# Kernel tuning notes

Hardware: AMD Instinct MI355X
Metric: run time of the kernel (lower is better)

## Reference

```python
import jax, jax.numpy as jnp
import numpy as np

NUM_USER, NUM_ITEM, K, B = 8192, 16384, 2048, 2048
LAMD0, CC, P = 40000.0, 5000.0, 0.5


def setup_inputs() -> dict:
    key = jax.random.key(0)
    ks = jax.random.split(key, 11)
    UI = (jax.random.uniform(ks[0], (NUM_USER, NUM_ITEM)) < 0.02).astype(jnp.float32)
    u = jax.random.normal(ks[1], (NUM_ITEM, K), dtype=jnp.float32) * 0.02
    s = jax.random.uniform(ks[2], (K,), dtype=jnp.float32) * 100.0 + 1.0  # positive singular values
    vh = jax.random.normal(ks[3], (K, NUM_ITEM), dtype=jnp.float32) * 0.02
    lamd_w = jnp.zeros((K, 1), jnp.float32)
    D_w = jnp.zeros((NUM_ITEM, 1), jnp.float32)
    Db_w = jnp.zeros((1, NUM_ITEM), jnp.float32)
    # dropout mask with keep prob 1-P, scaled by 1/(1-P) (torch training-mode Dropout)
    drop_mask = (jax.random.uniform(ks[4], (B, NUM_ITEM)) > P).astype(jnp.float32) / (1.0 - P)
    user = jax.random.randint(ks[5], (B,), 0, NUM_USER)
    pos_item = jax.random.randint(ks[6], (B,), 0, NUM_ITEM)
    neg_item = jax.random.randint(ks[7], (B,), 0, NUM_ITEM)
    return {"UI": UI, "u": u, "s": s, "vh": vh, "lamd_w": lamd_w, "D_w": D_w,
            "Db_w": Db_w, "drop_mask": drop_mask, "user": user,
            "pos_item": pos_item, "neg_item": neg_item}


def _gather_W_cols(u, ss, vh, dg, dbg, items):
    # Columns of W = sigmoid(D) * (u @ diag(ss) @ vh) * sigmoid(Db), diag zeroed.
    # Equivalent to original getW() followed by W[:, items], without materializing W.
    cols = u @ (ss[:, None] * vh[:, items])          # [num_item, Bi]
    cols = dg[:, None] * cols * dbg[items][None, :]  # row gate * col gate
    cols = cols.at[items, jnp.arange(items.shape[0])].set(0.0)  # W[i,i] = 0
    return cols.T                                    # [Bi, num_item]


def reference(UI, u, s, vh, lamd_w, D_w, Db_w, drop_mask, user, pos_item, neg_item):
    ss = s / (s + LAMD0 + CC * jnp.tanh(lamd_w[:, 0]))  # [K]
    dg = jax.nn.sigmoid(D_w[:, 0])    # [num_item] row gate
    dbg = jax.nn.sigmoid(Db_w[0])     # [num_item] col gate
    posW = _gather_W_cols(u, ss, vh, dg, dbg, pos_item)  # [B, num_item]
    negW = _gather_W_cols(u, ss, vh, dg, dbg, neg_item)  # [B, num_item]
    A = UI[user]                                          # [B, num_item]
    A = A.at[jnp.arange(user.shape[0]), pos_item].set(0.0)
    A = A * drop_mask
    pos = (A * posW).sum(1)
    neg = (A * negW).sum(1)
    loss = -jax.nn.log_sigmoid(100.0 * (pos - neg)).mean()
    return loss
```

## Files before the change

### kernel.cpp

```cpp
#include <hip/hip_runtime.h>
#include <hip/hip_bf16.h>
#include <math.h>

#define NUSER 8192
#define NITEM 16384
#define KD 2048
#define BB 2048

typedef __bf16 bf16;
typedef __bf16 bf16x8 __attribute__((ext_vector_type(8)));
typedef float f32x4 __attribute__((ext_vector_type(4)));

__global__ __launch_bounds__(256) void gates_kernel(
    const float* __restrict__ s, const float* __restrict__ lamd_w,
    const float* __restrict__ D_w, const float* __restrict__ Db_w,
    float* __restrict__ ss, float* __restrict__ dg, float* __restrict__ dbg) {
  int i = blockIdx.x * 256 + threadIdx.x;
  if (i < NITEM) {
    dg[i] = 1.0f / (1.0f + expf(-D_w[i]));
    dbg[i] = 1.0f / (1.0f + expf(-Db_w[i]));
    if (i < KD) {
      float sv = s[i];
      ss[i] = sv / (sv + 40000.0f + 5000.0f * tanhf(lamd_w[i]));
    }
  }
}

__global__ __launch_bounds__(256) void prep_a_kernel(
    const float* __restrict__ UI, const float* __restrict__ drop,
    const float* __restrict__ dg, const int* __restrict__ user,
    const int* __restrict__ pos_item, bf16* __restrict__ Ag) {
  int j = blockIdx.x;
  int t = threadIdx.x;
  int uj = user[j];
  int pj = pos_item[j];
  const float* uirow = UI + (size_t)uj * NITEM;
  const float* drow = drop + (size_t)j * NITEM;
  bf16* arow = Ag + (size_t)j * NITEM;
#pragma unroll
  for (int it = 0; it < 8; ++it) {
    int i = it * 2048 + t * 8;
    float4 a0 = *(const float4*)&uirow[i];
    float4 a1 = *(const float4*)&uirow[i + 4];
    float4 d0 = *(const float4*)&drow[i];
    float4 d1 = *(const float4*)&drow[i + 4];
    float4 g0 = *(const float4*)&dg[i];
    float4 g1 = *(const float4*)&dg[i + 4];
    float v[8] = {a0.x * d0.x * g0.x, a0.y * d0.y * g0.y, a0.z * d0.z * g0.z,
                  a0.w * d0.w * g0.w, a1.x * d1.x * g1.x, a1.y * d1.y * g1.y,
                  a1.z * d1.z * g1.z, a1.w * d1.w * g1.w};
    bf16x8 o;
#pragma unroll
    for (int w = 0; w < 8; ++w) o[w] = (bf16)((i + w == pj) ? 0.0f : v[w]);
    *(bf16x8*)&arow[i] = o;
  }
}

__global__ __launch_bounds__(256) void transpose_u_kernel(
    const float* __restrict__ u, bf16* __restrict__ Bt) {
  __shared__ bf16 ldsT[64][72];
  int i0 = blockIdx.x * 64;
  int k0 = blockIdx.y * 64;
  int t = threadIdx.x;
  int r = t >> 2, q = t & 3;
#pragma unroll
  for (int cc = 0; cc < 4; ++cc) {
    int col = q * 16 + cc * 4;
    float4 v = *(const float4*)&u[(size_t)(i0 + r) * KD + k0 + col];
    ldsT[col + 0][r] = (bf16)v.x;
    ldsT[col + 1][r] = (bf16)v.y;
    ldsT[col + 2][r] = (bf16)v.z;
    ldsT[col + 3][r] = (bf16)v.w;
  }
  __syncthreads();
#pragma unroll
  for (int g = 0; g < 2; ++g) {
    int ii = q * 16 + g * 8;
    bf16x8 v = *(const bf16x8*)&ldsT[r][ii];
    *(bf16x8*)&Bt[(size_t)(k0 + r) * NITEM + i0 + ii] = v;
  }
}

#define BM 128
#define BN 128
#define BKK 64

__global__ __launch_bounds__(256) void gemm_kernel(
    const bf16* __restrict__ A, const bf16* __restrict__ Bt,
    float* __restrict__ Y) {
  __shared__ bf16 lA[BM][BKK + 8];
  __shared__ bf16 lB[BN][BKK + 8];
  int bm = blockIdx.x * BM;
  int bn = blockIdx.y * BN;
  int kz = blockIdx.z;
  int tid = threadIdx.x;
  int wid = tid >> 6, lane = tid & 63;
  int wr = (wid >> 1) * 64, wc = (wid & 1) * 64;
  int lrow = lane & 15;
  int lko = (lane >> 4) * 8;
  f32x4 acc[4][4] = {};
  int kbeg = kz * (NITEM / 4), kend = kbeg + NITEM / 4;
  for (int kt = kbeg; kt < kend; kt += BKK) {
#pragma unroll
    for (int it = 0; it < 4; ++it) {
      int idx = tid + it * 256;
      int rr = idx >> 3, c8 = (idx & 7) * 8;
      *(bf16x8*)&lA[rr][c8] = *(const bf16x8*)&A[(size_t)(bm + rr) * NITEM + kt + c8];
      *(bf16x8*)&lB[rr][c8] = *(const bf16x8*)&Bt[(size_t)(bn + rr) * NITEM + kt + c8];
    }
    __syncthreads();
#pragma unroll
    for (int kk = 0; kk < BKK; kk += 32) {
      bf16x8 af[4], bfv[4];
#pragma unroll
      for (int m = 0; m < 4; ++m) af[m] = *(const bf16x8*)&lA[wr + m * 16 + lrow][kk + lko];
#pragma unroll
      for (int n = 0; n < 4; ++n) bfv[n] = *(const bf16x8*)&lB[wc + n * 16 + lrow][kk + lko];
#pragma unroll
      for (int m = 0; m < 4; ++m)
#pragma unroll
        for (int n = 0; n < 4; ++n)
          acc[m][n] = __builtin_amdgcn_mfma_f32_16x16x32_bf16(af[m], bfv[n], acc[m][n], 0, 0, 0);
    }
    __syncthreads();
  }
  int ccol = lane & 15, crow = (lane >> 4) * 4;
  float* yz = Y + (size_t)kz * BB * BB;
#pragma unroll
  for (int m = 0; m < 4; ++m)
#pragma unroll
    for (int n = 0; n < 4; ++n)
#pragma unroll
      for (int rix = 0; rix < 4; ++rix)
        yz[(size_t)(bm + wr + m * 16 + crow + rix) * BB + bn + wc + n * 16 + ccol] =
            acc[m][n][rix];
}

__global__ __launch_bounds__(256) void final_kernel(
    const float* __restrict__ Y, const float* __restrict__ ss,
    const float* __restrict__ dbg, const float* __restrict__ dg,
    const float* __restrict__ vh, const float* __restrict__ u,
    const float* __restrict__ UI, const float* __restrict__ drop,
    const int* __restrict__ user, const int* __restrict__ pos_item,
    const int* __restrict__ neg_item, float* __restrict__ out) {
  int j = blockIdx.x;
  int t = threadIdx.x;
  int pj = pos_item[j], nj = neg_item[j];
  float spos = 0.0f, sneg = 0.0f, sun = 0.0f;
#pragma unroll
  for (int it = 0; it < 8; ++it) {
    int k = it * 256 + t;
    float y = Y[(size_t)j * BB + k] + Y[(size_t)(BB + j) * BB + k] +
              Y[(size_t)(2 * BB + j) * BB + k] + Y[(size_t)(3 * BB + j) * BB + k];
    float sk = ss[k];
    float gp = sk * vh[(size_t)k * NITEM + pj];
    float gn = sk * vh[(size_t)k * NITEM + nj];
    spos += y * gp;
    sneg += y * gn;
    sun += u[(size_t)nj * KD + k] * gn;
  }
  for (int o = 32; o; o >>= 1) {
    spos += __shfl_down(spos, o, 64);
    sneg += __shfl_down(sneg, o, 64);
    sun += __shfl_down(sun, o, 64);
  }
  __shared__ float red[3][4];
  int wid = t >> 6;
  if ((t & 63) == 0) { red[0][wid] = spos; red[1][wid] = sneg; red[2][wid] = sun; }
  __syncthreads();
  if (t == 0) {
    spos = red[0][0] + red[0][1] + red[0][2] + red[0][3];
    sneg = red[1][0] + red[1][1] + red[1][2] + red[1][3];
    sun = red[2][0] + red[2][1] + red[2][2] + red[2][3];
    float adiag = (nj == pj) ? 0.0f
                             : UI[(size_t)user[j] * NITEM + nj] *
                                   drop[(size_t)j * NITEM + nj] * dg[nj];
    float pos = dbg[pj] * spos;
    float neg = dbg[nj] * (sneg - adiag * sun);
    float z = 100.0f * (pos - neg);
    float lossterm = (z >= 0.0f) ? log1pf(expf(-z)) : (-z + log1pf(expf(z)));
    atomicAdd(out, lossterm * (1.0f / (float)BB));
  }
}

extern "C" void kernel_launch(void* const* d_in, const int* in_sizes, int n_in,
                              void* d_out, int out_size, void* d_ws, size_t ws_size,
                              hipStream_t stream) {
  const float* UI = (const float*)d_in[0];
  const float* u = (const float*)d_in[1];
  const float* s = (const float*)d_in[2];
  const float* vh = (const float*)d_in[3];
  const float* lamd_w = (const float*)d_in[4];
  const float* D_w = (const float*)d_in[5];
  const float* Db_w = (const float*)d_in[6];
  const float* drop = (const float*)d_in[7];
  const int* user = (const int*)d_in[8];
  const int* pos_item = (const int*)d_in[9];
  const int* neg_item = (const int*)d_in[10];
  float* out = (float*)d_out;

  char* ws = (char*)d_ws;
  size_t off = 0;
  auto alloc = [&](size_t bytes) {
    void* p = ws + off;
    off = (off + bytes + 255) & ~(size_t)255;
    return p;
  };
  float* ss = (float*)alloc((size_t)KD * 4);
  float* dg = (float*)alloc((size_t)NITEM * 4);
  float* dbg = (float*)alloc((size_t)NITEM * 4);
  bf16* Ag = (bf16*)alloc((size_t)BB * NITEM * 2);
  bf16* Bt = (bf16*)alloc((size_t)KD * NITEM * 2);
  float* Y = (float*)alloc((size_t)4 * BB * BB * 4);

  hipMemsetAsync(d_out, 0, sizeof(float), stream);
  gates_kernel<<<NITEM / 256, 256, 0, stream>>>(s, lamd_w, D_w, Db_w, ss, dg, dbg);
  prep_a_kernel<<<BB, 256, 0, stream>>>(UI, drop, dg, user, pos_item, Ag);
  transpose_u_kernel<<<dim3(NITEM / 64, KD / 64), 256, 0, stream>>>(u, Bt);
  gemm_kernel<<<dim3(BB / BM, BB / BN, 4), 256, 0, stream>>>(Ag, Bt, Y);
  final_kernel<<<BB, 256, 0, stream>>>(Y, ss, dbg, dg, vh, u, UI, drop, user,
                                       pos_item, neg_item, out);
}
```

Baseline: 1.226 ms.

## Pre-transpose scaled vh for contiguous final gathers and use async LDS loads in GEMM

Adds a kernel that transposes vh into an item-major [NITEM, KD] buffer, with the ss scaling folded in. The final kernel then reads the pos/neg item columns as contiguous rows instead of strided single-element gathers across 2048 rows. Separately, the GEMM tile loads now use global_load_lds (direct global-to-LDS async copies), which requires dropping the LDS row padding. The trade-offs are an extra full read and write of the 128 MB vh matrix, possible LDS bank conflicts from the unpadded layout, and reliance on __syncthreads covering the async-copy completion.

```diff
diff --git a/kernel.cpp b/kernel.cpp
--- a/kernel.cpp
+++ b/kernel.cpp
@@ -10,6 +10,12 @@
 typedef __bf16 bf16;
 typedef __bf16 bf16x8 __attribute__((ext_vector_type(8)));
 typedef float f32x4 __attribute__((ext_vector_type(4)));
+
+__device__ __forceinline__ void async16(const bf16* g, bf16* l) {
+  __builtin_amdgcn_global_load_lds(
+      (const __attribute__((address_space(1))) void*)g,
+      (__attribute__((address_space(3))) void*)l, 16, 0, 0);
+}
 
 __global__ __launch_bounds__(256) void gates_kernel(
     const float* __restrict__ s, const float* __restrict__ lamd_w,
@@ -81,6 +87,37 @@
   }
 }
 
+__global__ __launch_bounds__(256) void transpose_vh_kernel(
+    const float* __restrict__ vh, const float* __restrict__ ss,
+    float* __restrict__ vhT) {
+  __shared__ float tile[64][65];
+  int i0 = blockIdx.x * 64;
+  int k0 = blockIdx.y * 64;
+  int t = threadIdx.x;
+  int r = t >> 4, c4 = (t & 15) * 4;
+#pragma unroll
+  for (int p = 0; p < 4; ++p) {
+    int row = p * 16 + r;
+    float4 v = *(const float4*)&vh[(size_t)(k0 + row) * NITEM + i0 + c4];
+    float sk = ss[k0 + row];
+    tile[c4 + 0][row] = v.x * sk;
+    tile[c4 + 1][row] = v.y * sk;
+    tile[c4 + 2][row] = v.z * sk;
+    tile[c4 + 3][row] = v.w * sk;
+  }
+  __syncthreads();
+#pragma unroll
+  for (int p = 0; p < 4; ++p) {
+    int row = p * 16 + r;
+    float4 o;
+    o.x = tile[row][c4 + 0];
+    o.y = tile[row][c4 + 1];
+    o.z = tile[row][c4 + 2];
+    o.w = tile[row][c4 + 3];
+    *(float4*)&vhT[(size_t)(i0 + row) * KD + k0 + c4] = o;
+  }
+}
+
 #define BM 128
 #define BN 128
 #define BKK 64
@@ -88,8 +125,8 @@
 __global__ __launch_bounds__(256) void gemm_kernel(
     const bf16* __restrict__ A, const bf16* __restrict__ Bt,
     float* __restrict__ Y) {
-  __shared__ bf16 lA[BM][BKK + 8];
-  __shared__ bf16 lB[BN][BKK + 8];
+  __shared__ bf16 lA[BM][BKK];
+  __shared__ bf16 lB[BN][BKK];
   int bm = blockIdx.x * BM;
   int bn = blockIdx.y * BN;
   int kz = blockIdx.z;
@@ -103,10 +140,11 @@
   for (int kt = kbeg; kt < kend; kt += BKK) {
 #pragma unroll
     for (int it = 0; it < 4; ++it) {
-      int idx = tid + it * 256;
+      int idx = it * 256 + tid;
       int rr = idx >> 3, c8 = (idx & 7) * 8;
-      *(bf16x8*)&lA[rr][c8] = *(const bf16x8*)&A[(size_t)(bm + rr) * NITEM + kt + c8];
-      *(bf16x8*)&lB[rr][c8] = *(const bf16x8*)&Bt[(size_t)(bn + rr) * NITEM + kt + c8];
+      int base = it * 256 + (tid & ~63);
+      async16(&A[(size_t)(bm + rr) * NITEM + kt + c8], &((bf16*)lA)[(size_t)base * 8]);
+      async16(&Bt[(size_t)(bn + rr) * NITEM + kt + c8], &((bf16*)lB)[(size_t)base * 8]);
     }
     __syncthreads();
 #pragma unroll
@@ -137,27 +175,29 @@
 }
 
 __global__ __launch_bounds__(256) void final_kernel(
-    const float* __restrict__ Y, const float* __restrict__ ss,
+    const float* __restrict__ Y, const float* __restrict__ vhT,
     const float* __restrict__ dbg, const float* __restrict__ dg,
-    const float* __restrict__ vh, const float* __restrict__ u,
-    const float* __restrict__ UI, const float* __restrict__ drop,
-    const int* __restrict__ user, const int* __restrict__ pos_item,
-    const int* __restrict__ neg_item, float* __restrict__ out) {
+    const float* __restrict__ u, const float* __restrict__ UI,
+    const float* __restrict__ drop, const int* __restrict__ user,
+    const int* __restrict__ pos_item, const int* __restrict__ neg_item,
+    float* __restrict__ out) {
   int j = blockIdx.x;
   int t = threadIdx.x;
   int pj = pos_item[j], nj = neg_item[j];
+  const float* vp = vhT + (size_t)pj * KD;
+  const float* vn = vhT + (size_t)nj * KD;
+  const float* un = u + (size_t)nj * KD;
   float spos = 0.0f, sneg = 0.0f, sun = 0.0f;
 #pragma unroll
   for (int it = 0; it < 8; ++it) {
     int k = it * 256 + t;
     float y = Y[(size_t)j * BB + k] + Y[(size_t)(BB + j) * BB + k] +
               Y[(size_t)(2 * BB + j) * BB + k] + Y[(size_t)(3 * BB + j) * BB + k];
-    float sk = ss[k];
-    float gp = sk * vh[(size_t)k * NITEM + pj];
-    float gn = sk * vh[(size_t)k * NITEM + nj];
+    float gp = vp[k];
+    float gn = vn[k];
     spos += y * gp;
     sneg += y * gn;
-    sun += u[(size_t)nj * KD + k] * gn;
+    sun += un[k] * gn;
   }
   for (int o = 32; o; o >>= 1) {
     spos += __shfl_down(spos, o, 64);
@@ -212,12 +252,14 @@
   bf16* Ag = (bf16*)alloc((size_t)BB * NITEM * 2);
   bf16* Bt = (bf16*)alloc((size_t)KD * NITEM * 2);
   float* Y = (float*)alloc((size_t)4 * BB * BB * 4);
+  float* vhT = (float*)alloc((size_t)NITEM * KD * 4);
 
   hipMemsetAsync(d_out, 0, sizeof(float), stream);
   gates_kernel<<<NITEM / 256, 256, 0, stream>>>(s, lamd_w, D_w, Db_w, ss, dg, dbg);
   prep_a_kernel<<<BB, 256, 0, stream>>>(UI, drop, dg, user, pos_item, Ag);
   transpose_u_kernel<<<dim3(NITEM / 64, KD / 64), 256, 0, stream>>>(u, Bt);
+  transpose_vh_kernel<<<dim3(NITEM / 64, KD / 64), 256, 0, stream>>>(vh, ss, vhT);
   gemm_kernel<<<dim3(BB / BM, BB / BN, 4), 256, 0, stream>>>(Ag, Bt, Y);
-  final_kernel<<<BB, 256, 0, stream>>>(Y, ss, dbg, dg, vh, u, UI, drop, user,
+  final_kernel<<<BB, 256, 0, stream>>>(Y, vhT, dbg, dg, u, UI, drop, user,
                                        pos_item, neg_item, out);
 }
```

Measured after the change: 1.170 ms. 4.6% less time.
